# Performance work log

Measured on AMD Instinct MI355X. Metric: run time of the kernel, lower is better.

Reference implementation:

```python
import jax, jax.numpy as jnp
import numpy as np

E = 1024      # hidden_size
H = 16        # num_heads
D = E // H    # head_dim = 64
WIN = 256     # window_size
STRIDE = 128
G = 1         # global_tokens
B = 2
L = 4097      # seq_len; local_seq_len = 4096 tiles exactly into 31 windows


def setup_inputs() -> dict:
    key = jax.random.key(0)
    ks = jax.random.split(key, 9)
    s = 0.02
    return {
        "hidden_states": jax.random.normal(ks[0], (B, L, E), jnp.float32),
        "Wq": jax.random.normal(ks[1], (E, E), jnp.float32) * s,
        "bq": jnp.zeros((E,), jnp.float32),
        "Wk": jax.random.normal(ks[2], (E, E), jnp.float32) * s,
        "bk": jnp.zeros((E,), jnp.float32),
        "Wv": jax.random.normal(ks[3], (E, E), jnp.float32) * s,
        "bv": jnp.zeros((E,), jnp.float32),
        "Wo": jax.random.normal(ks[4], (E, E), jnp.float32) * s,
        "bo": jnp.zeros((E,), jnp.float32),
    }


def reference(hidden_states, Wq, bq, Wk, bk, Wv, bv, Wo, bo):
    b, seq_len, e = hidden_states.shape
    scale = 1.0 / jnp.sqrt(jnp.asarray(D, hidden_states.dtype))

    q = (hidden_states @ Wq + bq).reshape(b, seq_len, H, D)
    k = (hidden_states @ Wk + bk).reshape(b, seq_len, H, D)
    v = (hidden_states @ Wv + bv).reshape(b, seq_len, H, D)

    # ---- global tokens attend to the full sequence ----
    qg = q[:, :G]                                        # [b, G, H, D]
    gw = jnp.einsum('bghd,bshd->bhgs', qg, k) * scale    # [b, H, G, L]
    gp = jax.nn.softmax(gw, axis=-1)
    gctx = jnp.einsum('bhgs,bshd->bghd', gp, v).reshape(b, G, e)

    # ---- local windowed attention (overlapping strided windows) ----
    ql, kl, vl = q[:, G:], k[:, G:], v[:, G:]
    Lc = seq_len - G                                     # 4096
    num_windows = max(1, (Lc - WIN) // STRIDE + 1)       # 31
    starts = jnp.arange(num_windows) * STRIDE
    widx = starts[:, None] + jnp.arange(WIN)             # [W, w] window indices

    qw = ql[:, widx]                                     # [b, W, w, H, D]
    kw = kl[:, widx]
    vw = vl[:, widx]
    aw = jnp.einsum('bwqhd,bwkhd->bwhqk', qw, kw) * scale  # [b, W, H, w, w]
    ap = jax.nn.softmax(aw, axis=-1)
    ctx = jnp.einsum('bwhqk,bwkhd->bwqhd', ap, vw)       # [b, W, w, H, D]
    ctx = ctx.reshape(b, num_windows * WIN, e)

    flat = widx.reshape(-1)                              # [W*w]
    local = jnp.zeros((b, Lc, e), hidden_states.dtype).at[:, flat].add(ctx)
    counts = jnp.zeros((Lc,), hidden_states.dtype).at[flat].add(1.0)
    counts = jnp.maximum(counts, 1.0)
    local = local / counts[None, :, None]                # average over overlaps

    out = jnp.concatenate([gctx, local], axis=1)         # [b, L, E]
    return out @ Wo + bo
```

## Files before the change

kernel.cpp:

```cpp
#include <hip/hip_runtime.h>

typedef unsigned short u16;
typedef unsigned int u32;
typedef __bf16 bf16x8 __attribute__((ext_vector_type(8)));
typedef float f4_t __attribute__((ext_vector_type(4)));

#define E_DIM 1024
#define L_TOT 4097
#define B_SZ 2
#define M_ROWS 8194
#define NWIN 31
#define HHEADS 16
#define GCHUNKS 17

__device__ __forceinline__ float b2f(u16 v) {
  union { u32 u; float f; } x; x.u = ((u32)v) << 16; return x.f;
}
__device__ __forceinline__ u16 f2b(float f) {
  union { float f; u32 u; } x; x.f = f;
  u32 r = (x.u + 0x7FFFu + ((x.u >> 16) & 1u)) >> 16;
  return (u16)r;
}
__device__ __forceinline__ f4_t mfma16(bf16x8 a, bf16x8 b, f4_t c) {
  return __builtin_amdgcn_mfma_f32_16x16x32_bf16(a, b, c, 0, 0, 0);
}
__device__ __forceinline__ u32 cvtpk(float lo, float hi) {
  u32 r;
  asm volatile("v_cvt_pk_bf16_f32 %0, %1, %2" : "=v"(r) : "v"(lo), "v"(hi));
  return r;
}

#define GLOAD16(gp, lp)                                                              \
  __builtin_amdgcn_global_load_lds(                                                  \
      (const __attribute__((address_space(1))) u32*)(gp),                            \
      (__attribute__((address_space(3))) u32*)(lp), 16, 0, 0)

__global__ __launch_bounds__(256) void cvt_kernel(const float* __restrict__ src,
                                                  u16* __restrict__ dst, int n4) {
  int i = blockIdx.x * 256 + threadIdx.x;
  if (i >= n4) return;
  float4 v = ((const float4*)src)[i];
  u16 o[4] = {f2b(v.x), f2b(v.y), f2b(v.z), f2b(v.w)};
  *(uint2*)(dst + (size_t)i * 4) = *(uint2*)o;
}

__global__ __launch_bounds__(256) void wtrans_kernel(const float* __restrict__ w0,
                                                     const float* __restrict__ w1,
                                                     const float* __restrict__ w2,
                                                     const float* __restrict__ w3,
                                                     u16* __restrict__ wtb) {
  const float* src = blockIdx.z == 0 ? w0 : blockIdx.z == 1 ? w1 : blockIdx.z == 2 ? w2 : w3;
  u16* dst = wtb + (size_t)blockIdx.z * E_DIM * E_DIM;
  __shared__ float tile[32][33];
  int tx = threadIdx.x, ty = threadIdx.y;
  int x = blockIdx.x * 32 + tx;
  int y0 = blockIdx.y * 32;
  for (int j = ty; j < 32; j += 8) tile[j][tx] = src[(size_t)(y0 + j) * E_DIM + x];
  __syncthreads();
  for (int j = ty; j < 32; j += 8)
    dst[(size_t)(blockIdx.x * 32 + j) * E_DIM + blockIdx.y * 32 + tx] = f2b(tile[tx][j]);
}

template <int MODE, int BN>
__global__ __launch_bounds__(256) void gemmB_kernel(const u16* __restrict__ A,
                                                    const u16* __restrict__ Wt,
                                                    const float* __restrict__ b0,
                                                    const float* __restrict__ b1,
                                                    const float* __restrict__ b2,
                                                    void* __restrict__ outBase,
                                                    int M, int NTIL) {
  constexpr int NB = BN / 32;
  constexpr int ABUF = 128 * 64;
  constexpr int BBUF = BN * 64;
  __shared__ __align__(16) u16 sm[2 * ABUF + 2 * BBUF];
  u16* sA = sm;
  u16* sB = sm + 2 * ABUF;
  u16* epi16 = sm;
  float* epi32 = (float*)sm;

  int nwg = gridDim.x;
  int q8 = nwg >> 3, r8 = nwg & 7;
  int orig = blockIdx.x;
  int xcd = orig & 7, loc = orig >> 3;
  int wg = (xcd < r8 ? xcd * (q8 + 1) : r8 * (q8 + 1) + (xcd - r8) * q8) + loc;
  int mt = wg / NTIL, nt = wg - mt * NTIL;
  int m0 = mt * 128, n0 = nt * BN;

  int t = threadIdx.x, lane = t & 63, w = t >> 6;
  int wr = w >> 1, wc = w & 1;
  int lr = lane & 15, g = lane >> 4;

  int rsub = t >> 3;
  int ssrc = ((t & 7) ^ (rsub & 7)) * 8;
  int wbase = w * 512;
  const u16* pa[4];
  const u16* pb[NB];
#pragma unroll
  for (int c = 0; c < 4; c++) {
    int ra = m0 + c * 32 + rsub;
    if (ra >= M) ra = M - 1;
    pa[c] = A + (size_t)ra * 1024 + ssrc;
  }
#pragma unroll
  for (int c = 0; c < NB; c++) pb[c] = Wt + (size_t)(n0 + c * 32 + rsub) * 1024 + ssrc;

#define STAGE(bf, kt)                                                      \
  {                                                                        \
    int ko_ = (kt) * 64;                                                   \
    _Pragma("unroll") for (int c_ = 0; c_ < 4; c_++)                       \
        GLOAD16(pa[c_] + ko_, sA + (bf) * ABUF + c_ * 2048 + wbase);       \
    _Pragma("unroll") for (int c_ = 0; c_ < NB; c_++)                      \
        GLOAD16(pb[c_] + ko_, sB + (bf) * BBUF + c_ * 2048 + wbase);       \
  }

#define COMPUTE(bf)                                                            \
  {                                                                            \
    _Pragma("unroll") for (int kk_ = 0; kk_ < 2; kk_++) {                      \
      int sl_ = ((kk_ * 4 + g) ^ (lr & 7)) * 8;                                \
      bf16x8 av_[4], bv_[NB];                                                  \
      _Pragma("unroll") for (int i_ = 0; i_ < 4; i_++)                         \
          av_[i_] = *(const bf16x8*)&sA[(bf) * ABUF + (wr * 64 + i_ * 16 + lr) * 64 + sl_]; \
      _Pragma("unroll") for (int j_ = 0; j_ < NB; j_++)                        \
          bv_[j_] = *(const bf16x8*)&sB[(bf) * BBUF + (wc * (BN / 2) + j_ * 16 + lr) * 64 + sl_]; \
      _Pragma("unroll") for (int i_ = 0; i_ < 4; i_++)                         \
        _Pragma("unroll") for (int j_ = 0; j_ < NB; j_++)                      \
            acc[i_][j_] = mfma16(av_[i_], bv_[j_], acc[i_][j_]);               \
    }                                                                          \
  }

  f4_t acc[4][NB] = {};

  STAGE(0, 0);
  __syncthreads();

  int buf = 0;
  for (int kt = 0; kt < 15; ++kt) {
    STAGE(buf ^ 1, kt + 1);
    __builtin_amdgcn_sched_barrier(0);
    COMPUTE(buf);
    __syncthreads();
    buf ^= 1;
  }
  COMPUTE(buf);
  __syncthreads();

  if (MODE == 0) {
    int tsel = n0 >> 10, ncb = n0 & 1023;
    const float* bp = tsel == 0 ? b0 : (tsel == 1 ? b1 : b2);
#pragma unroll
    for (int j = 0; j < NB; j++) {
      int ncl = wc * (BN / 2) + j * 16 + lr;
      float bb = bp[ncb + ncl];
#pragma unroll
      for (int i = 0; i < 4; i++) {
        int mlb = wr * 64 + i * 16 + g * 4;
#pragma unroll
        for (int r = 0; r < 4; r++) epi16[(mlb + r) * 136 + ncl] = f2b(acc[i][j][r] + bb);
      }
    }
    __syncthreads();
    int row = t >> 1, half = t & 1;
    int m = m0 + row;
    if (m < M) {
      u16* op = (u16*)outBase + (size_t)tsel * ((size_t)M_ROWS * E_DIM) + (size_t)m * E_DIM + ncb + half * 64;
      const u16* lp = epi16 + row * 136 + half * 64;
#pragma unroll
      for (int qd = 0; qd < 8; qd++) ((uint4*)op)[qd] = ((const uint4*)lp)[qd];
    }
  } else {
#pragma unroll
    for (int j = 0; j < NB; j++) {
      int ncl = wc * (BN / 2) + j * 16 + lr;
      float bb = b0[n0 + ncl];
#pragma unroll
      for (int i = 0; i < 4; i++) {
        int mlb = wr * 64 + i * 16 + g * 4;
#pragma unroll
        for (int r = 0; r < 4; r++) epi32[(mlb + r) * 68 + ncl] = acc[i][j][r] + bb;
      }
    }
    __syncthreads();
    int row = t >> 1, half = t & 1;
    int m = m0 + row;
    if (m < M) {
      float* op = (float*)outBase + (size_t)m * E_DIM + n0 + half * 32;
      const float* lp = epi32 + row * 68 + half * 32;
#pragma unroll
      for (int qd = 0; qd < 8; qd++) ((float4*)op)[qd] = ((const float4*)lp)[qd];
    }
  }
#undef STAGE
#undef COMPUTE
}

__global__ __launch_bounds__(256) void gattn1_kernel(const u16* __restrict__ Qb,
                                                     const u16* __restrict__ Kb,
                                                     const u16* __restrict__ Vb,
                                                     float* __restrict__ part) {
  int c = blockIdx.x;
  int h = blockIdx.y;
  int b = blockIdx.z;
  int t = threadIdx.x;
  __shared__ float qsh[64];
  __shared__ float red[4];
  __shared__ float psh[256];
  __shared__ float cred[4][64];

  size_t base = (size_t)b * L_TOT * E_DIM + h * 64;
  if (t < 64) qsh[t] = b2f(Qb[base + t]);
  __syncthreads();

  int row = c * 256 + t;
  bool valid = row < L_TOT;
  float dot = -1e30f;
  if (valid) {
    const u16* kp = Kb + base + (size_t)row * E_DIM;
    float acc = 0.f;
#pragma unroll
    for (int j = 0; j < 64; j += 8) {
      uint4 kv = *(const uint4*)(kp + j);
      const u16* kk = (const u16*)&kv;
#pragma unroll
      for (int q = 0; q < 8; q++) acc += qsh[j + q] * b2f(kk[q]);
    }
    dot = acc * 0.125f;
  }
  float m = dot;
  for (int mask = 1; mask < 64; mask <<= 1) m = fmaxf(m, __shfl_xor(m, mask));
  if ((t & 63) == 0) red[t >> 6] = m;
  __syncthreads();
  m = fmaxf(fmaxf(red[0], red[1]), fmaxf(red[2], red[3]));
  float p = valid ? __expf(dot - m) : 0.f;
  psh[t] = p;
  float s = p;
  for (int mask = 1; mask < 64; mask <<= 1) s += __shfl_xor(s, mask);
  __syncthreads();
  if ((t & 63) == 0) red[t >> 6] = s;
  __syncthreads();
  s = red[0] + red[1] + red[2] + red[3];

  int d = t & 63, gq = t >> 6;
  float acc = 0.f;
#pragma unroll 4
  for (int i = 0; i < 64; i++) {
    int sl = gq * 64 + i;
    int r2 = c * 256 + sl;
    if (r2 < L_TOT) acc += psh[sl] * b2f(Vb[base + (size_t)r2 * E_DIM + d]);
  }
  cred[gq][d] = acc;
  __syncthreads();
  if (t < 64) {
    float v = cred[0][t] + cred[1][t] + cred[2][t] + cred[3][t];
    float* pp = part + (((size_t)(b * HHEADS + h) * GCHUNKS + c) * 66);
    pp[t] = v;
    if (t == 0) { pp[64] = m; pp[65] = s; }
  }
}

__global__ __launch_bounds__(64) void gattn2_kernel(const float* __restrict__ part,
                                                    u16* __restrict__ ctxb) {
  int bh = blockIdx.x;
  int b = bh >> 4, h = bh & 15;
  int d = threadIdx.x;
  const float* pp = part + ((size_t)(b * HHEADS + h) * GCHUNKS) * 66;
  float m = -1e30f;
#pragma unroll
  for (int c = 0; c < GCHUNKS; c++) m = fmaxf(m, pp[c * 66 + 64]);
  float stot = 0.f, acc = 0.f;
#pragma unroll
  for (int c = 0; c < GCHUNKS; c++) {
    float w = __expf(pp[c * 66 + 64] - m);
    stot += pp[c * 66 + 65] * w;
    acc += pp[c * 66 + d] * w;
  }
  ctxb[(size_t)b * L_TOT * E_DIM + h * 64 + d] = f2b(acc / stot);
}

#define VT_IDX(d, k) ((d) * 264 + ((k) ^ ((((d) >> 3) & 7) << 3)))
__global__ __launch_bounds__(256) void wattn_kernel(const u16* __restrict__ Qb,
                                                    const u16* __restrict__ Kb,
                                                    const u16* __restrict__ Vb,
                                                    u16* __restrict__ winctx) {
  int wdw = blockIdx.x;
  int h = blockIdx.y;
  int b = blockIdx.z;

  __shared__ __align__(16) u16 Ks[256 * 64];
  __shared__ __align__(16) u16 Vt[64 * 264];

  int t = threadIdx.x, lane = t & 63, wv = t >> 6;
  int g = lane >> 4, lr = lane & 15;
  size_t rowbase = (size_t)b * L_TOT + 1 + (size_t)wdw * 128;
  int hoff = h * 64;

  {
    int rsub = t >> 3;
    int ssrc = ((t & 7) ^ (rsub & 7)) * 8;
    const u16* kp = Kb + (rowbase + rsub) * E_DIM + hoff + ssrc;
#pragma unroll
    for (int c = 0; c < 8; c++)
      GLOAD16(kp + (size_t)c * 32 * E_DIM, Ks + c * 2048 + wv * 512);
  }
#pragma unroll
  for (int rep = 0; rep < 8; rep++) {
    int u = rep * 256 + t;
    int i = u >> 3;
    int d0 = (u & 7) * 8;
    uint4 v = *(const uint4*)(Vb + (rowbase + i) * E_DIM + hoff + d0);
    const u16* pv = (const u16*)&v;
#pragma unroll
    for (int j = 0; j < 8; j++) Vt[VT_IDX(d0 + j, i)] = pv[j];
  }
  __syncthreads();

  int slo = (2 * (g & 1)) * 16 + lr;
  int shi = slo + 16;

  for (int grp = 0; grp < 4; grp++) {
    int q0 = grp * 64 + wv * 16;
    const u16* qp = Qb + (rowbase + q0 + lr) * E_DIM + hoff;
    bf16x8 qa0 = *(const bf16x8*)(qp + g * 8);
    bf16x8 qa1 = *(const bf16x8*)(qp + 32 + g * 8);

    f4_t s[16];
    __builtin_amdgcn_s_setprio(1);
#pragma unroll
    for (int ki = 0; ki < 16; ki++) {
      int row = ki * 16 + lr;
      bf16x8 ka0 = *(const bf16x8*)&Ks[row * 64 + ((g ^ (lr & 7)) << 3)];
      bf16x8 ka1 = *(const bf16x8*)&Ks[row * 64 + (((4 + g) ^ (lr & 7)) << 3)];
      f4_t z = {};
      z = mfma16(ka0, qa0, z);
      z = mfma16(ka1, qa1, z);
      s[ki] = z;
    }
    __builtin_amdgcn_s_setprio(0);

    float mx = -1e30f;
#pragma unroll
    for (int ki = 0; ki < 16; ki++) {
      mx = fmaxf(mx, fmaxf(fmaxf(s[ki][0], s[ki][1]), fmaxf(s[ki][2], s[ki][3])));
    }
    mx = fmaxf(mx, __shfl_xor(mx, 16));
    mx = fmaxf(mx, __shfl_xor(mx, 32));
    float mx8 = mx * 0.125f;
    float sum = 0.f;
    u32 pk[16][2];
#pragma unroll
    for (int ki = 0; ki < 16; ki++) {
      float p0 = __expf(fmaf(s[ki][0], 0.125f, -mx8));
      float p1 = __expf(fmaf(s[ki][1], 0.125f, -mx8));
      float p2 = __expf(fmaf(s[ki][2], 0.125f, -mx8));
      float p3 = __expf(fmaf(s[ki][3], 0.125f, -mx8));
      sum += (p0 + p1) + (p2 + p3);
      pk[ki][0] = cvtpk(p0, p1);
      pk[ki][1] = cvtpk(p2, p3);
    }
    sum += __shfl_xor(sum, 16);
    sum += __shfl_xor(sum, 32);
    float inv = 1.0f / sum;

    u32 paw[8][4];
    bool hi = g >= 2;
#pragma unroll
    for (int kt = 0; kt < 8; kt++) {
      u32 v00 = __shfl((int)pk[kt * 2][0], slo);
      u32 v01 = __shfl((int)pk[kt * 2][1], slo);
      u32 v10 = __shfl((int)pk[kt * 2 + 1][0], slo);
      u32 v11 = __shfl((int)pk[kt * 2 + 1][1], slo);
      u32 w00 = __shfl((int)pk[kt * 2][0], shi);
      u32 w01 = __shfl((int)pk[kt * 2][1], shi);
      u32 w10 = __shfl((int)pk[kt * 2 + 1][0], shi);
      u32 w11 = __shfl((int)pk[kt * 2 + 1][1], shi);
      paw[kt][0] = hi ? v10 : v00;
      paw[kt][1] = hi ? v11 : v01;
      paw[kt][2] = hi ? w10 : w00;
      paw[kt][3] = hi ? w11 : w01;
    }

    f4_t o[4] = {};
    __builtin_amdgcn_s_setprio(1);
#pragma unroll
    for (int dtile = 0; dtile < 4; dtile++) {
      int d = dtile * 16 + lr;
      int dswz = (((d >> 3) & 7) << 3);
#pragma unroll
      for (int kt = 0; kt < 8; kt++) {
        int kphys = (kt * 32 + g * 8) ^ dswz;
        bf16x8 vb = *(const bf16x8*)&Vt[d * 264 + kphys];
        o[dtile] = mfma16(*(const bf16x8*)&paw[kt][0], vb, o[dtile]);
      }
    }
    __builtin_amdgcn_s_setprio(0);

    float invr[4];
#pragma unroll
    for (int r = 0; r < 4; r++) invr[r] = __shfl(inv, g * 4 + r);
    size_t orow = (size_t)(b * NWIN + wdw) * 256 + q0;
#pragma unroll
    for (int dtile = 0; dtile < 4; dtile++) {
#pragma unroll
      for (int r = 0; r < 4; r++) {
        winctx[(orow + g * 4 + r) * E_DIM + hoff + dtile * 16 + lr] =
            f2b(o[dtile][r] * invr[r]);
      }
    }
  }
}

__global__ __launch_bounds__(256) void combine_kernel(const u16* __restrict__ winctx,
                                                      u16* __restrict__ ctxb) {
  int idx = blockIdx.x * 256 + threadIdx.x;
  int e0 = (idx & 127) * 8;
  int p = (idx >> 7) & 4095;
  int b = idx >> 19;
  int whi = p >> 7;
  if (whi > 30) whi = 30;
  int off_hi = p - whi * 128;
  int wlo = whi - 1;
  bool has_lo = (wlo >= 0) && (off_hi < 128);

  uint4 vhi = *(const uint4*)(winctx + (((size_t)(b * NWIN + whi) * 256 + off_hi) * E_DIM) + e0);
  const u16* ph = (const u16*)&vhi;
  float vals[8];
#pragma unroll
  for (int j = 0; j < 8; j++) vals[j] = b2f(ph[j]);
  if (has_lo) {
    uint4 vlo = *(const uint4*)(winctx + (((size_t)(b * NWIN + wlo) * 256 + off_hi + 128) * E_DIM) + e0);
    const u16* pl = (const u16*)&vlo;
#pragma unroll
    for (int j = 0; j < 8; j++) vals[j] = (vals[j] + b2f(pl[j])) * 0.5f;
  }
  u16 out[8];
#pragma unroll
  for (int j = 0; j < 8; j++) out[j] = f2b(vals[j]);
  *(uint4*)(ctxb + ((size_t)b * L_TOT + 1 + p) * E_DIM + e0) = *(uint4*)out;
}

extern "C" void kernel_launch(void* const* d_in, const int* in_sizes, int n_in,
                              void* d_out, int out_size, void* d_ws, size_t ws_size,
                              hipStream_t stream) {
  const float* hs = (const float*)d_in[0];
  const float* Wq = (const float*)d_in[1];
  const float* bq = (const float*)d_in[2];
  const float* Wk = (const float*)d_in[3];
  const float* bk = (const float*)d_in[4];
  const float* Wv = (const float*)d_in[5];
  const float* bv = (const float*)d_in[6];
  const float* Wo = (const float*)d_in[7];
  const float* bo = (const float*)d_in[8];

  const size_t BLE = (size_t)M_ROWS * E_DIM;
  const size_t BLE_B = BLE * 2;
  const size_t EE = (size_t)E_DIM * E_DIM;

  char* ws = (char*)d_ws;
  u16* hsb = (u16*)(ws);
  u16* wtb = (u16*)(ws + BLE_B);
  u16* qkv = (u16*)(ws + BLE_B + 4 * EE * 2);
  u16* Qb = qkv;
  u16* Kb = qkv + BLE;
  u16* Vb = qkv + 2 * BLE;
  u16* ctxb = (u16*)(ws + BLE_B + 4 * EE * 2 + 3 * BLE_B);
  u16* winctx = (u16*)(ws + BLE_B + 4 * EE * 2 + 4 * BLE_B);
  float* gpart = (float*)(ws + BLE_B + 4 * EE * 2 + 4 * BLE_B +
                          (size_t)B_SZ * NWIN * 256 * E_DIM * 2);

  cvt_kernel<<<8194, 256, 0, stream>>>(hs, hsb, (int)(BLE / 4));
  wtrans_kernel<<<dim3(32, 32, 4), dim3(32, 8), 0, stream>>>(Wq, Wk, Wv, Wo, wtb);
  gemmB_kernel<0, 128><<<65 * 24, 256, 0, stream>>>(hsb, wtb, bq, bk, bv, qkv, M_ROWS, 24);
  gattn1_kernel<<<dim3(GCHUNKS, HHEADS, B_SZ), 256, 0, stream>>>(Qb, Kb, Vb, gpart);
  gattn2_kernel<<<32, 64, 0, stream>>>(gpart, ctxb);
  wattn_kernel<<<dim3(NWIN, HHEADS, B_SZ), 256, 0, stream>>>(Qb, Kb, Vb, winctx);
  combine_kernel<<<4096, 256, 0, stream>>>(winctx, ctxb);
  gemmB_kernel<1, 64><<<65 * 16, 256, 0, stream>>>(ctxb, wtb + 3 * EE, bo, bo, bo, d_out, M_ROWS, 16);
}
```

Measured before the change: 226.0 us.

## Replace bf16 GEMM with 256x256-tile 8-wave ping-pong scheduled kernel

Replaces the 128xBN 4-wave double-buffered GEMM with a 512-thread kernel that computes 256x256 output tiles. The K loop is split into half-K phases: each phase interleaves direct-to-LDS global loads with MFMA work, using explicit vmcnt waits, s_barrier and raised wave priority around the MFMA bursts. The aim is more data reuse per tile and better overlap of loads with compute. In exchange the grids become much smaller (396 and 132 workgroups), which risks leaving CUs idle and adds tail imbalance. The fp32 output epilogue now writes straight from registers instead of staging through LDS.

After: 218.8 us. -3.2%, faster.

```diff
diff --git a/kernel.cpp b/kernel.cpp
--- a/kernel.cpp
+++ b/kernel.cpp
@@ -34,6 +34,14 @@
   __builtin_amdgcn_global_load_lds(                                                  \
       (const __attribute__((address_space(1))) u32*)(gp),                            \
       (__attribute__((address_space(3))) u32*)(lp), 16, 0, 0)
+
+#define WAITVM(N) asm volatile("s_waitcnt vmcnt(" #N ")" ::: "memory")
+#define SBAR                                  \
+  {                                           \
+    __builtin_amdgcn_sched_barrier(0);        \
+    __builtin_amdgcn_s_barrier();             \
+    __builtin_amdgcn_sched_barrier(0);        \
+  }
 
 __global__ __launch_bounds__(256) void cvt_kernel(const float* __restrict__ src,
                                                   u16* __restrict__ dst, int n4) {
@@ -61,22 +69,20 @@
     dst[(size_t)(blockIdx.x * 32 + j) * E_DIM + blockIdx.y * 32 + tx] = f2b(tile[tx][j]);
 }
 
-template <int MODE, int BN>
-__global__ __launch_bounds__(256) void gemmB_kernel(const u16* __restrict__ A,
-                                                    const u16* __restrict__ Wt,
-                                                    const float* __restrict__ b0,
-                                                    const float* __restrict__ b1,
-                                                    const float* __restrict__ b2,
-                                                    void* __restrict__ outBase,
-                                                    int M, int NTIL) {
-  constexpr int NB = BN / 32;
-  constexpr int ABUF = 128 * 64;
-  constexpr int BBUF = BN * 64;
-  __shared__ __align__(16) u16 sm[2 * ABUF + 2 * BBUF];
+template <int MODE>
+__global__ __launch_bounds__(512, 1) void gemm8_kernel(const u16* __restrict__ A,
+                                                       const u16* __restrict__ Wt,
+                                                       const float* __restrict__ b0,
+                                                       const float* __restrict__ b1,
+                                                       const float* __restrict__ b2,
+                                                       void* __restrict__ outBase,
+                                                       int M, int NTIL) {
+  constexpr int AHALF = 256 * 32;
+  constexpr int ABUF = 2 * AHALF;
+  __shared__ __align__(16) u16 sm[4 * ABUF];
   u16* sA = sm;
   u16* sB = sm + 2 * ABUF;
-  u16* epi16 = sm;
-  float* epi32 = (float*)sm;
+  u16* epi = sm;
 
   int nwg = gridDim.x;
   int q8 = nwg >> 3, r8 = nwg & 7;
@@ -84,113 +90,173 @@
   int xcd = orig & 7, loc = orig >> 3;
   int wg = (xcd < r8 ? xcd * (q8 + 1) : r8 * (q8 + 1) + (xcd - r8) * q8) + loc;
   int mt = wg / NTIL, nt = wg - mt * NTIL;
-  int m0 = mt * 128, n0 = nt * BN;
+  int m0 = mt * 256, n0 = nt * 256;
 
   int t = threadIdx.x, lane = t & 63, w = t >> 6;
-  int wr = w >> 1, wc = w & 1;
+  int wm = w >> 2, wn = w & 3;
   int lr = lane & 15, g = lane >> 4;
 
-  int rsub = t >> 3;
-  int ssrc = ((t & 7) ^ (rsub & 7)) * 8;
-  int wbase = w * 512;
-  const u16* pa[4];
-  const u16* pb[NB];
-#pragma unroll
-  for (int c = 0; c < 4; c++) {
-    int ra = m0 + c * 32 + rsub;
+  int ssrc = (((t & 3) ^ ((t >> 3) & 3)) << 3);
+  const u16* paA[2];
+  const u16* pbB[2];
+#pragma unroll
+  for (int i = 0; i < 2; i++) {
+    int ra = m0 + i * 128 + (t >> 2);
     if (ra >= M) ra = M - 1;
-    pa[c] = A + (size_t)ra * 1024 + ssrc;
-  }
-#pragma unroll
-  for (int c = 0; c < NB; c++) pb[c] = Wt + (size_t)(n0 + c * 32 + rsub) * 1024 + ssrc;
-
-#define STAGE(bf, kt)                                                      \
-  {                                                                        \
-    int ko_ = (kt) * 64;                                                   \
-    _Pragma("unroll") for (int c_ = 0; c_ < 4; c_++)                       \
-        GLOAD16(pa[c_] + ko_, sA + (bf) * ABUF + c_ * 2048 + wbase);       \
-    _Pragma("unroll") for (int c_ = 0; c_ < NB; c_++)                      \
-        GLOAD16(pb[c_] + ko_, sB + (bf) * BBUF + c_ * 2048 + wbase);       \
-  }
-
-#define COMPUTE(bf)                                                            \
-  {                                                                            \
-    _Pragma("unroll") for (int kk_ = 0; kk_ < 2; kk_++) {                      \
-      int sl_ = ((kk_ * 4 + g) ^ (lr & 7)) * 8;                                \
-      bf16x8 av_[4], bv_[NB];                                                  \
-      _Pragma("unroll") for (int i_ = 0; i_ < 4; i_++)                         \
-          av_[i_] = *(const bf16x8*)&sA[(bf) * ABUF + (wr * 64 + i_ * 16 + lr) * 64 + sl_]; \
-      _Pragma("unroll") for (int j_ = 0; j_ < NB; j_++)                        \
-          bv_[j_] = *(const bf16x8*)&sB[(bf) * BBUF + (wc * (BN / 2) + j_ * 16 + lr) * 64 + sl_]; \
-      _Pragma("unroll") for (int i_ = 0; i_ < 4; i_++)                         \
-        _Pragma("unroll") for (int j_ = 0; j_ < NB; j_++)                      \
-            acc[i_][j_] = mfma16(av_[i_], bv_[j_], acc[i_][j_]);               \
-    }                                                                          \
-  }
-
-  f4_t acc[4][NB] = {};
-
-  STAGE(0, 0);
-  __syncthreads();
-
-  int buf = 0;
-  for (int kt = 0; kt < 15; ++kt) {
-    STAGE(buf ^ 1, kt + 1);
-    __builtin_amdgcn_sched_barrier(0);
-    COMPUTE(buf);
-    __syncthreads();
-    buf ^= 1;
-  }
-  COMPUTE(buf);
+    paA[i] = A + (size_t)ra * 1024 + ssrc;
+    pbB[i] = Wt + (size_t)(n0 + i * 128 + (t >> 2)) * 1024 + ssrc;
+  }
+  int wb = w * 512;
+
+#define STA(bf, kh, kt)                                                          \
+  {                                                                              \
+    GLOAD16(paA[0] + (kt) * 64 + (kh) * 32, sA + (bf) * ABUF + (kh) * AHALF + wb);       \
+    GLOAD16(paA[1] + (kt) * 64 + (kh) * 32, sA + (bf) * ABUF + (kh) * AHALF + 4096 + wb); \
+  }
+#define STB(bf, kh, kt)                                                          \
+  {                                                                              \
+    GLOAD16(pbB[0] + (kt) * 64 + (kh) * 32, sB + (bf) * ABUF + (kh) * AHALF + wb);       \
+    GLOAD16(pbB[1] + (kt) * 64 + (kh) * 32, sB + (bf) * ABUF + (kh) * AHALF + 4096 + wb); \
+  }
+
+  int swz = ((g ^ ((lr >> 1) & 3)) << 3);
+  int arow0 = wm * 128 + lr;
+  int brow0 = wn * 64 + lr;
+
+#define RD_A(bf, KK, MH, mi) \
+  (*(const bf16x8*)&sA[(bf) * ABUF + (KK) * AHALF + (arow0 + (MH) * 64 + (mi) * 16) * 32 + swz])
+#define RD_B(bf, KK, nj) \
+  (*(const bf16x8*)&sB[(bf) * ABUF + (KK) * AHALF + (brow0 + (nj) * 16) * 32 + swz])
+
+  f4_t acc[8][4] = {};
+  bf16x8 bvr0, bvr1, bvr2, bvr3;
+
+#define MMROW(MH, mi, af)                                    \
+  acc[(MH) * 4 + (mi)][0] = mfma16(af, bvr0, acc[(MH) * 4 + (mi)][0]); \
+  acc[(MH) * 4 + (mi)][1] = mfma16(af, bvr1, acc[(MH) * 4 + (mi)][1]); \
+  acc[(MH) * 4 + (mi)][2] = mfma16(af, bvr2, acc[(MH) * 4 + (mi)][2]); \
+  acc[(MH) * 4 + (mi)][3] = mfma16(af, bvr3, acc[(MH) * 4 + (mi)][3]);
+
+#define PHASE(bf, MH, KK, LOADB, STG)                        \
+  {                                                          \
+    bf16x8 af0 = RD_A(bf, KK, MH, 0);                        \
+    bf16x8 af1 = RD_A(bf, KK, MH, 1);                        \
+    bf16x8 af2 = RD_A(bf, KK, MH, 2);                        \
+    bf16x8 af3 = RD_A(bf, KK, MH, 3);                        \
+    if (LOADB) {                                             \
+      bvr0 = RD_B(bf, KK, 0);                                \
+      bvr1 = RD_B(bf, KK, 1);                                \
+      bvr2 = RD_B(bf, KK, 2);                                \
+      bvr3 = RD_B(bf, KK, 3);                                \
+    }                                                        \
+    STG;                                                     \
+    SBAR;                                                    \
+    __builtin_amdgcn_s_setprio(1);                           \
+    MMROW(MH, 0, af0);                                       \
+    MMROW(MH, 1, af1);                                       \
+    MMROW(MH, 2, af2);                                       \
+    MMROW(MH, 3, af3);                                       \
+    __builtin_amdgcn_s_setprio(0);                           \
+  }
+
+  STA(0, 0, 0); STB(0, 0, 0);
+  STA(0, 1, 0); STB(0, 1, 0);
+  STA(1, 0, 1); STB(1, 0, 1);
+
+  for (int j = 0; j < 7; ++j) {
+    int k1 = 2 * j + 1, k2 = 2 * j + 2, k3 = 2 * j + 3;
+    WAITVM(4);
+    SBAR;
+    PHASE(0, 0, 0, true, STA(1, 1, k1));
+    SBAR;
+    PHASE(0, 1, 0, false, STB(1, 1, k1));
+    SBAR;
+    PHASE(0, 0, 1, true, STA(0, 0, k2));
+    SBAR;
+    PHASE(0, 1, 1, false, STB(0, 0, k2));
+    WAITVM(4);
+    SBAR;
+    PHASE(1, 0, 0, true, STA(0, 1, k2));
+    SBAR;
+    PHASE(1, 1, 0, false, STB(0, 1, k2));
+    SBAR;
+    PHASE(1, 0, 1, true, STA(1, 0, k3));
+    SBAR;
+    PHASE(1, 1, 1, false, STB(1, 0, k3));
+  }
+  {
+    WAITVM(4);
+    SBAR;
+    PHASE(0, 0, 0, true, STA(1, 1, 15));
+    SBAR;
+    PHASE(0, 1, 0, false, STB(1, 1, 15));
+    SBAR;
+    PHASE(0, 0, 1, true, {});
+    SBAR;
+    PHASE(0, 1, 1, false, {});
+    WAITVM(0);
+    SBAR;
+    PHASE(1, 0, 0, true, {});
+    SBAR;
+    PHASE(1, 1, 0, false, {});
+    SBAR;
+    PHASE(1, 0, 1, true, {});
+    SBAR;
+    PHASE(1, 1, 1, false, {});
+  }
   __syncthreads();
 
   if (MODE == 0) {
     int tsel = n0 >> 10, ncb = n0 & 1023;
     const float* bp = tsel == 0 ? b0 : (tsel == 1 ? b1 : b2);
-#pragma unroll
-    for (int j = 0; j < NB; j++) {
-      int ncl = wc * (BN / 2) + j * 16 + lr;
-      float bb = bp[ncb + ncl];
-#pragma unroll
-      for (int i = 0; i < 4; i++) {
-        int mlb = wr * 64 + i * 16 + g * 4;
-#pragma unroll
-        for (int r = 0; r < 4; r++) epi16[(mlb + r) * 136 + ncl] = f2b(acc[i][j][r] + bb);
+    u16* outp = (u16*)outBase + (size_t)tsel * ((size_t)M_ROWS * E_DIM);
+#pragma unroll
+    for (int h = 0; h < 2; ++h) {
+      if (h) __syncthreads();
+      if (wm == h) {
+#pragma unroll
+        for (int nj = 0; nj < 4; nj++) {
+          int cl = wn * 64 + nj * 16 + lr;
+          float bb = bp[ncb + cl];
+#pragma unroll
+          for (int mi = 0; mi < 8; mi++) {
+#pragma unroll
+            for (int r = 0; r < 4; r++)
+              epi[(mi * 16 + g * 4 + r) * 264 + cl] = f2b(acc[mi][nj][r] + bb);
+          }
+        }
       }
-    }
-    __syncthreads();
-    int row = t >> 1, half = t & 1;
-    int m = m0 + row;
-    if (m < M) {
-      u16* op = (u16*)outBase + (size_t)tsel * ((size_t)M_ROWS * E_DIM) + (size_t)m * E_DIM + ncb + half * 64;
-      const u16* lp = epi16 + row * 136 + half * 64;
-#pragma unroll
-      for (int qd = 0; qd < 8; qd++) ((uint4*)op)[qd] = ((const uint4*)lp)[qd];
+      __syncthreads();
+      int row = t >> 2, c0 = (t & 3) * 64;
+      int m = m0 + h * 128 + row;
+      if (m < M) {
+        u16* op = outp + (size_t)m * E_DIM + ncb + c0;
+        const u16* lp = epi + row * 264 + c0;
+#pragma unroll
+        for (int qd = 0; qd < 8; qd++) ((uint4*)op)[qd] = ((const uint4*)lp)[qd];
+      }
     }
   } else {
-#pragma unroll
-    for (int j = 0; j < NB; j++) {
-      int ncl = wc * (BN / 2) + j * 16 + lr;
-      float bb = b0[n0 + ncl];
-#pragma unroll
-      for (int i = 0; i < 4; i++) {
-        int mlb = wr * 64 + i * 16 + g * 4;
-#pragma unroll
-        for (int r = 0; r < 4; r++) epi32[(mlb + r) * 68 + ncl] = acc[i][j][r] + bb;
+    float* outp = (float*)outBase;
+#pragma unroll
+    for (int nj = 0; nj < 4; nj++) {
+      int n = n0 + wn * 64 + nj * 16 + lr;
+      float bb = b0[n];
+#pragma unroll
+      for (int mi = 0; mi < 8; mi++) {
+        int mb = m0 + wm * 128 + mi * 16 + g * 4;
+#pragma unroll
+        for (int r = 0; r < 4; r++)
+          if (mb + r < M) outp[(size_t)(mb + r) * E_DIM + n] = acc[mi][nj][r] + bb;
       }
     }
-    __syncthreads();
-    int row = t >> 1, half = t & 1;
-    int m = m0 + row;
-    if (m < M) {
-      float* op = (float*)outBase + (size_t)m * E_DIM + n0 + half * 32;
-      const float* lp = epi32 + row * 68 + half * 32;
-#pragma unroll
-      for (int qd = 0; qd < 8; qd++) ((float4*)op)[qd] = ((const float4*)lp)[qd];
-    }
-  }
-#undef STAGE
-#undef COMPUTE
+  }
+#undef STA
+#undef STB
+#undef RD_A
+#undef RD_B
+#undef MMROW
+#undef PHASE
 }
 
 __global__ __launch_bounds__(256) void gattn1_kernel(const u16* __restrict__ Qb,
@@ -468,10 +534,10 @@
 
   cvt_kernel<<<8194, 256, 0, stream>>>(hs, hsb, (int)(BLE / 4));
   wtrans_kernel<<<dim3(32, 32, 4), dim3(32, 8), 0, stream>>>(Wq, Wk, Wv, Wo, wtb);
-  gemmB_kernel<0, 128><<<65 * 24, 256, 0, stream>>>(hsb, wtb, bq, bk, bv, qkv, M_ROWS, 24);
+  gemm8_kernel<0><<<33 * 12, 512, 0, stream>>>(hsb, wtb, bq, bk, bv, qkv, M_ROWS, 12);
   gattn1_kernel<<<dim3(GCHUNKS, HHEADS, B_SZ), 256, 0, stream>>>(Qb, Kb, Vb, gpart);
   gattn2_kernel<<<32, 64, 0, stream>>>(gpart, ctxb);
   wattn_kernel<<<dim3(NWIN, HHEADS, B_SZ), 256, 0, stream>>>(Qb, Kb, Vb, winctx);
   combine_kernel<<<4096, 256, 0, stream>>>(winctx, ctxb);
-  gemmB_kernel<1, 64><<<65 * 16, 256, 0, stream>>>(ctxb, wtb + 3 * EE, bo, bo, bo, d_out, M_ROWS, 16);
-}
+  gemm8_kernel<1><<<33 * 4, 512, 0, stream>>>(ctxb, wtb + 3 * EE, bo, bo, bo, d_out, M_ROWS, 4);
+}
```
